# Kernel tuning notes

Measured on AMD Instinct MI355X. Metric: run time of the kernel, lower is better.

## Reference

```python
import jax, jax.numpy as jnp
from jax import lax
import numpy as np

EPS_REG = 1.0     # ot.sinkhorn(..., M, 1, ...) hardcodes reg=1 in the original forward
N_ITER = 100      # max_iter: fixed stabilized (log-domain) Sinkhorn iterations


def setup_inputs() -> dict:
    key = jax.random.key(0)
    kx, ky = jax.random.split(key)
    x = jax.random.normal(kx, (1, 4096, 512), dtype=jnp.float32)
    y = jax.random.normal(ky, (1, 4096, 512), dtype=jnp.float32)
    return {"x": x, "y": y}


def _cost_matrix(x, y):
    x2 = jnp.sum(x * x, axis=-1)                      # [B, P1]
    y2 = jnp.sum(y * y, axis=-1)                      # [B, P2]
    xy = jnp.einsum("bpd,bqd->bpq", x, y)            # [B, P1, P2]
    return jnp.maximum(x2[:, :, None] + y2[:, None, :] - 2.0 * xy, 0.0)


def _sinkhorn_log(C, eps, n_iter):
    # Log-domain (stabilized) Sinkhorn with uniform marginals a=1/P1, b=1/P2.
    P1, P2 = C.shape
    eps_loga = eps * (-jnp.log(jnp.float32(P1)))
    eps_logb = eps * (-jnp.log(jnp.float32(P2)))

    def step(carry, _):
        f, g = carry
        f = eps_loga - eps * jax.nn.logsumexp((g[None, :] - C) / eps, axis=1)
        g = eps_logb - eps * jax.nn.logsumexp((f[:, None] - C) / eps, axis=0)
        return (f, g), None

    f0 = jnp.zeros((P1,), C.dtype)
    g0 = jnp.zeros((P2,), C.dtype)
    (f, g), _ = lax.scan(step, (f0, g0), None, length=n_iter)
    return jnp.exp((f[:, None] + g[None, :] - C) / eps)  # transport plan pi, rows sum to 1/P1


def reference(x, y):
    C = _cost_matrix(x, y)                                  # [B, P1, P2]
    pi = jax.vmap(lambda c: _sinkhorn_log(c, EPS_REG, N_ITER))(C)
    cost = jnp.sum(pi * C, axis=(-2, -1))                   # [B], reduction='none'
    return cost, pi, C
```

## Files before the change

kernel.cpp:

```cpp
#include <hip/hip_runtime.h>
#include <hip/hip_bf16.h>
#include <cstddef>

#define NROW 4096
#define DIM  512
static const size_t NP = (size_t)NROW * NROW;
#define L2E   1.4426950408889634f
#define ALPHA2 (-12.0f)
#define QSCALE 64.0f
#define QD    (1.4426950408889634f / 64.0f)

typedef unsigned int uint32;

__global__ __launch_bounds__(256) void sqnorm_kernel(const float* __restrict__ x,
                                                     const float* __restrict__ y,
                                                     float* __restrict__ x2,
                                                     float* __restrict__ y2) {
    int gtid = blockIdx.x * 256 + threadIdx.x;
    int wid  = gtid >> 6;
    int lane = gtid & 63;
    const float* src = (wid < NROW) ? x : y;
    float*       dst = (wid < NROW) ? x2 : y2;
    int row = (wid < NROW) ? wid : (wid - NROW);
    const float4* r4 = (const float4*)(src + (size_t)row * DIM);
    float4 a = r4[lane];
    float4 b = r4[lane + 64];
    float s = a.x*a.x + a.y*a.y + a.z*a.z + a.w*a.w
            + b.x*b.x + b.y*b.y + b.z*b.z + b.w*b.w;
    #pragma unroll
    for (int off = 32; off > 0; off >>= 1) s += __shfl_down(s, off);
    if (lane == 0) dst[row] = s;
}

__global__ __launch_bounds__(256) void gemm_kernel(const float* __restrict__ A,
                                                   const float* __restrict__ B,
                                                   float* __restrict__ S) {
    __shared__ float As[16][132];
    __shared__ float Bs[16][132];
    const int bm = blockIdx.y * 128, bn = blockIdx.x * 128;
    const int tid = threadIdx.x;
    const int tx = tid & 15, ty = tid >> 4;
    float acc[8][8];
    #pragma unroll
    for (int i = 0; i < 8; ++i)
        #pragma unroll
        for (int j = 0; j < 8; ++j) acc[i][j] = 0.f;

    for (int kt = 0; kt < DIM; kt += 16) {
        #pragma unroll
        for (int h = 0; h < 2; ++h) {
            int f = tid + h * 256;
            int row = f >> 2, kk = (f & 3) << 2;
            float4 a4 = *(const float4*)(A + (size_t)(bm + row) * DIM + kt + kk);
            As[kk+0][row] = a4.x; As[kk+1][row] = a4.y;
            As[kk+2][row] = a4.z; As[kk+3][row] = a4.w;
            float4 b4 = *(const float4*)(B + (size_t)(bn + row) * DIM + kt + kk);
            Bs[kk+0][row] = b4.x; Bs[kk+1][row] = b4.y;
            Bs[kk+2][row] = b4.z; Bs[kk+3][row] = b4.w;
        }
        __syncthreads();
        #pragma unroll
        for (int k = 0; k < 16; ++k) {
            float ar[8], br[8];
            #pragma unroll
            for (int i = 0; i < 8; ++i) ar[i] = As[k][ty*8 + i];
            #pragma unroll
            for (int j = 0; j < 8; ++j) br[j] = Bs[k][tx*8 + j];
            #pragma unroll
            for (int i = 0; i < 8; ++i)
                #pragma unroll
                for (int j = 0; j < 8; ++j)
                    acc[i][j] = __fmaf_rn(ar[i], br[j], acc[i][j]);
        }
        __syncthreads();
    }
    #pragma unroll
    for (int i = 0; i < 8; ++i) {
        size_t off = (size_t)(bm + ty*8 + i) * NROW + bn + tx*8;
        #pragma unroll
        for (int j = 0; j < 8; ++j) S[off + j] = 2.0f * acc[i][j];
    }
}

__global__ __launch_bounds__(256) void quantA_kernel(const float* __restrict__ S,
                                                     uint32* __restrict__ Sq) {
    size_t i = (size_t)blockIdx.x * 256 + threadIdx.x;
    const size_t nu = NP / 2, stride = (size_t)2048 * 256;
    for (; i < nu; i += stride) {
        float a = S[2*i], b = S[2*i + 1];
        float qa = fmaxf(fminf(a * QSCALE,  32767.f), -32767.f);
        float qb = fmaxf(fminf(b * QSCALE,  32767.f), -32767.f);
        int ia = __float2int_rn(qa), ib = __float2int_rn(qb);
        Sq[i] = (uint32)(ia & 0xffff) | ((uint32)ib << 16);
    }
}

__global__ __launch_bounds__(256) void quantT_kernel(const float* __restrict__ S,
                                                     uint32* __restrict__ SqT) {
    __shared__ short tile[64][66];
    const int bx = blockIdx.x * 64, by = blockIdx.y * 64;
    const int t = threadIdx.x;
    const int c = t & 63, r0 = t >> 6;
    #pragma unroll
    for (int rr = 0; rr < 16; ++rr) {
        int r = r0 + rr * 4;
        float v = S[(size_t)(by + r) * NROW + bx + c];
        float q = fmaxf(fminf(v * QSCALE, 32767.f), -32767.f);
        tile[r][c] = (short)__float2int_rn(q);
    }
    __syncthreads();
    const int p = t & 31, jl = t >> 5;
    #pragma unroll
    for (int jj = 0; jj < 8; ++jj) {
        int j = jj * 8 + jl;
        uint32 lo = (unsigned short)tile[2*p    ][j];
        uint32 hi = (unsigned short)tile[2*p + 1][j];
        SqT[(size_t)(bx + j) * (NROW/2) + (by >> 1) + p] = lo | (hi << 16);
    }
}

__global__ void init_kernel(const float* __restrict__ y2,
                            float* __restrict__ gt2,
                            float* __restrict__ cost) {
    int i = blockIdx.x * 256 + threadIdx.x;
    if (i < NROW) gt2[i] = -y2[i] * L2E;
    if (i == 0) cost[0] = 0.f;
}

__global__ __launch_bounds__(256) void lseq_kernel(const uint32* __restrict__ Q,
                                                   const float* __restrict__ u2,
                                                   float* __restrict__ o2) {
    const int r0 = blockIdx.x * 2;
    const uint32* q0 = Q + (size_t)r0 * (NROW/2);
    const uint32* q1 = q0 + (NROW/2);
    const int t = threadIdx.x;
    float m0 = -1e30f, s0 = 0.f, m1 = -1e30f, s1 = 0.f;
    #pragma unroll
    for (int h = 0; h < 8; ++h) {
        int k = t + h * 256;
        float2 uu = *(const float2*)(u2 + 2*k);
        uint32 w0 = q0[k], w1 = q1[k];
        float a0 = (float)(int)(short)(w0 & 0xffffu);
        float b0 = (float)((int)w0 >> 16);
        float a1 = (float)(int)(short)(w1 & 0xffffu);
        float b1 = (float)((int)w1 >> 16);
        float v00 = fmaf(a0, QD, uu.x), v01 = fmaf(b0, QD, uu.y);
        float v10 = fmaf(a1, QD, uu.x), v11 = fmaf(b1, QD, uu.y);
        float vm0 = fmaxf(v00, v01), vm1 = fmaxf(v10, v11);
        if (__any(vm0 > m0 + 60.f)) {
            float mn = fmaxf(m0, vm0);
            s0 *= exp2f(m0 - mn); m0 = mn;
        }
        if (__any(vm1 > m1 + 60.f)) {
            float mn = fmaxf(m1, vm1);
            s1 *= exp2f(m1 - mn); m1 = mn;
        }
        s0 += exp2f(v00 - m0) + exp2f(v01 - m0);
        s1 += exp2f(v10 - m1) + exp2f(v11 - m1);
    }
    #pragma unroll
    for (int off = 1; off < 64; off <<= 1) {
        float mo = __shfl_xor(m0, off), so = __shfl_xor(s0, off);
        float d = m0 - mo;
        float e = exp2f(-fabsf(d));
        s0 = (d > 0.f) ? fmaf(so, e, s0) : fmaf(s0, e, so);
        m0 = fmaxf(m0, mo);
        float mo1 = __shfl_xor(m1, off), so1 = __shfl_xor(s1, off);
        float d1 = m1 - mo1;
        float e1 = exp2f(-fabsf(d1));
        s1 = (d1 > 0.f) ? fmaf(so1, e1, s1) : fmaf(s1, e1, so1);
        m1 = fmaxf(m1, mo1);
    }
    __shared__ float sm0[4], ss0[4], sm1[4], ss1[4];
    int lane = t & 63, w = t >> 6;
    if (lane == 0) { sm0[w] = m0; ss0[w] = s0; sm1[w] = m1; ss1[w] = s1; }
    __syncthreads();
    if (t == 0) {
        float M0 = sm0[0], S0 = ss0[0], M1 = sm1[0], S1 = ss1[0];
        #pragma unroll
        for (int ww = 1; ww < 4; ++ww) {
            float d = M0 - sm0[ww];
            float e = exp2f(-fabsf(d));
            S0 = (d > 0.f) ? fmaf(ss0[ww], e, S0) : fmaf(S0, e, ss0[ww]);
            M0 = fmaxf(M0, sm0[ww]);
            float d1 = M1 - sm1[ww];
            float e1 = exp2f(-fabsf(d1));
            S1 = (d1 > 0.f) ? fmaf(ss1[ww], e1, S1) : fmaf(S1, e1, ss1[ww]);
            M1 = fmaxf(M1, sm1[ww]);
        }
        o2[r0]     = ALPHA2 - (M0 + __log2f(S0));
        o2[r0 + 1] = ALPHA2 - (M1 + __log2f(S1));
    }
}

__global__ __launch_bounds__(256) void finalize_kernel(const float* __restrict__ S,
                                                       const float* __restrict__ ft2,
                                                       const float* __restrict__ gt2,
                                                       const float* __restrict__ x2,
                                                       const float* __restrict__ y2,
                                                       float* __restrict__ pi,
                                                       float* __restrict__ C,
                                                       float* __restrict__ cost) {
    const int row = blockIdx.x;
    const size_t base = (size_t)row * NROW;
    const float fi2 = ft2[row];
    const float x2i = x2[row];
    float acc = 0.f;
    #pragma unroll
    for (int h = 0; h < 16; ++h) {
        int j = threadIdx.x + h * 256;
        float sv = S[base + j];
        float p  = exp2f(fmaf(sv, L2E, fi2 + gt2[j]));
        float c  = fmaxf(x2i + y2[j] - sv, 0.f);
        pi[base + j] = p;
        C[base + j]  = c;
        acc = __fmaf_rn(p, c, acc);
    }
    #pragma unroll
    for (int off = 32; off > 0; off >>= 1) acc += __shfl_down(acc, off);
    __shared__ float sa[4];
    int lane = threadIdx.x & 63, w = threadIdx.x >> 6;
    if (lane == 0) sa[w] = acc;
    __syncthreads();
    if (threadIdx.x == 0)
        atomicAdd(cost, sa[0] + sa[1] + sa[2] + sa[3]);
}

extern "C" void kernel_launch(void* const* d_in, const int* in_sizes, int n_in,
                              void* d_out, int out_size, void* d_ws, size_t ws_size,
                              hipStream_t stream) {
    const float* x = (const float*)d_in[0];
    const float* y = (const float*)d_in[1];
    float* out  = (float*)d_out;
    float* cost = out;
    float* pi   = out + 1;
    float* Cpt  = out + 1 + NP;
    float* S    = Cpt;
    uint32* Sq  = (uint32*)pi;
    uint32* SqT = Sq + NP/2;

    float* ws  = (float*)d_ws;
    float* x2  = ws;
    float* y2  = ws + NROW;
    float* ft2 = ws + 2 * NROW;
    float* gt2 = ws + 3 * NROW;

    sqnorm_kernel<<<2048, 256, 0, stream>>>(x, y, x2, y2);
    gemm_kernel<<<dim3(32, 32), 256, 0, stream>>>(x, y, S);
    quantA_kernel<<<2048, 256, 0, stream>>>(S, Sq);
    quantT_kernel<<<dim3(64, 64), 256, 0, stream>>>(S, SqT);
    init_kernel<<<16, 256, 0, stream>>>(y2, gt2, cost);

    for (int it = 0; it < 100; ++it) {
        lseq_kernel<<<2048, 256, 0, stream>>>(Sq,  gt2, ft2);
        lseq_kernel<<<2048, 256, 0, stream>>>(SqT, ft2, gt2);
    }

    finalize_kernel<<<NROW, 256, 0, stream>>>(S, ft2, gt2, x2, y2, pi, Cpt, cost);
}
```

Before: 2.921 ms.

## Fuse Sinkhorn iterations into one persistent cooperative kernel with grid sync

```diff
diff --git a/kernel.cpp b/kernel.cpp
--- a/kernel.cpp
+++ b/kernel.cpp
@@ -1,14 +1,19 @@
 #include <hip/hip_runtime.h>
-#include <hip/hip_bf16.h>
+#include <hip/hip_cooperative_groups.h>
 #include <cstddef>
+
+namespace cg = cooperative_groups;
 
 #define NROW 4096
 #define DIM  512
 static const size_t NP = (size_t)NROW * NROW;
-#define L2E   1.4426950408889634f
+#define L2E    1.4426950408889634f
 #define ALPHA2 (-12.0f)
 #define QSCALE 64.0f
-#define QD    (1.4426950408889634f / 64.0f)
+#define QD     (1.4426950408889634f / 64.0f)
+#define NBLK   256
+#define TPB    1024
+#define RPB    16
 
 typedef unsigned int uint32;
 
@@ -83,7 +88,9 @@
 }
 
 __global__ __launch_bounds__(256) void quantA_kernel(const float* __restrict__ S,
-                                                     uint32* __restrict__ Sq) {
+                                                     uint32* __restrict__ Sq,
+                                                     float* __restrict__ cost) {
+    if (blockIdx.x == 0 && threadIdx.x == 0) cost[0] = 0.f;
     size_t i = (size_t)blockIdx.x * 256 + threadIdx.x;
     const size_t nu = NP / 2, stride = (size_t)2048 * 256;
     for (; i < nu; i += stride) {
@@ -120,11 +127,68 @@
 }
 
 __global__ void init_kernel(const float* __restrict__ y2,
-                            float* __restrict__ gt2,
-                            float* __restrict__ cost) {
+                            float* __restrict__ gt2) {
     int i = blockIdx.x * 256 + threadIdx.x;
     if (i < NROW) gt2[i] = -y2[i] * L2E;
-    if (i == 0) cost[0] = 0.f;
+}
+
+__device__ __forceinline__ void lse_phase(const uint32* __restrict__ Q,
+                                          const float* __restrict__ u2,
+                                          float* __restrict__ o2,
+                                          float* __restrict__ u0, float* __restrict__ u1,
+                                          float* __restrict__ us2, float* __restrict__ u3,
+                                          int r0, int t, int w, int lane) {
+    {
+        float4 v = ((const float4*)u2)[t];
+        u0[t] = v.x; u1[t] = v.y; us2[t] = v.z; u3[t] = v.w;
+    }
+    __syncthreads();
+    const uint2* q2 = (const uint2*)(Q + (size_t)(r0 + w) * (NROW/2));
+    float m = -1e30f, s = 0.f;
+    #pragma unroll 4
+    for (int h = 0; h < 16; ++h) {
+        int k2 = lane + h * 64;
+        uint2 wv = q2[k2];
+        float a0 = (float)(int)(short)(wv.x & 0xffffu);
+        float b0 = (float)((int)wv.x >> 16);
+        float a1 = (float)(int)(short)(wv.y & 0xffffu);
+        float b1 = (float)((int)wv.y >> 16);
+        float v0 = fmaf(a0, QD, u0[k2]);
+        float v1 = fmaf(b0, QD, u1[k2]);
+        float v2 = fmaf(a1, QD, us2[k2]);
+        float v3 = fmaf(b1, QD, u3[k2]);
+        float vm = fmaxf(fmaxf(v0, v1), fmaxf(v2, v3));
+        if (__any(vm > m + 60.f)) {
+            float mn = fmaxf(m, vm);
+            s *= exp2f(m - mn); m = mn;
+        }
+        s += (exp2f(v0 - m) + exp2f(v1 - m)) + (exp2f(v2 - m) + exp2f(v3 - m));
+    }
+    #pragma unroll
+    for (int off = 1; off < 64; off <<= 1) {
+        float mo = __shfl_xor(m, off), so = __shfl_xor(s, off);
+        float d = m - mo;
+        float e = exp2f(-fabsf(d));
+        s = (d > 0.f) ? fmaf(so, e, s) : fmaf(s, e, so);
+        m = fmaxf(m, mo);
+    }
+    if (lane == 0) o2[r0 + w] = ALPHA2 - (m + __log2f(s));
+}
+
+__global__ __launch_bounds__(1024) void sink_iter_kernel(
+        const uint32* __restrict__ Sq, const uint32* __restrict__ SqT,
+        float* __restrict__ ft2, float* __restrict__ gt2) {
+    cg::grid_group grid = cg::this_grid();
+    __shared__ float u0[1024], u1[1024], us2[1024], u3[1024];
+    const int t = threadIdx.x;
+    const int w = t >> 6, lane = t & 63;
+    const int r0 = blockIdx.x * RPB;
+    for (int it = 0; it < 100; ++it) {
+        lse_phase(Sq,  gt2, ft2, u0, u1, us2, u3, r0, t, w, lane);
+        grid.sync();
+        lse_phase(SqT, ft2, gt2, u0, u1, us2, u3, r0, t, w, lane);
+        grid.sync();
+    }
 }
 
 __global__ __launch_bounds__(256) void lseq_kernel(const uint32* __restrict__ Q,
@@ -135,7 +199,7 @@
     const uint32* q1 = q0 + (NROW/2);
     const int t = threadIdx.x;
     float m0 = -1e30f, s0 = 0.f, m1 = -1e30f, s1 = 0.f;
-    #pragma unroll
+    #pragma unroll 2
     for (int h = 0; h < 8; ++h) {
         int k = t + h * 256;
         float2 uu = *(const float2*)(u2 + 2*k);
@@ -247,13 +311,19 @@
 
     sqnorm_kernel<<<2048, 256, 0, stream>>>(x, y, x2, y2);
     gemm_kernel<<<dim3(32, 32), 256, 0, stream>>>(x, y, S);
-    quantA_kernel<<<2048, 256, 0, stream>>>(S, Sq);
+    quantA_kernel<<<2048, 256, 0, stream>>>(S, Sq, cost);
     quantT_kernel<<<dim3(64, 64), 256, 0, stream>>>(S, SqT);
-    init_kernel<<<16, 256, 0, stream>>>(y2, gt2, cost);
-
-    for (int it = 0; it < 100; ++it) {
-        lseq_kernel<<<2048, 256, 0, stream>>>(Sq,  gt2, ft2);
-        lseq_kernel<<<2048, 256, 0, stream>>>(SqT, ft2, gt2);
+    init_kernel<<<16, 256, 0, stream>>>(y2, gt2);
+
+    void* kargs[] = { (void*)&Sq, (void*)&SqT, (void*)&ft2, (void*)&gt2 };
+    hipError_t cerr = hipLaunchCooperativeKernel((void*)sink_iter_kernel,
+                                                 dim3(NBLK), dim3(TPB),
+                                                 kargs, 0, stream);
+    if (cerr != hipSuccess) {
+        for (int it = 0; it < 100; ++it) {
+            lseq_kernel<<<2048, 256, 0, stream>>>(Sq,  gt2, ft2);
+            lseq_kernel<<<2048, 256, 0, stream>>>(SqT, ft2, gt2);
+        }
     }
 
     finalize_kernel<<<NROW, 256, 0, stream>>>(S, ft2, gt2, x2, y2, pi, Cpt, cost);
```

New measurement: 7.297 ms. +149.8%, slower.
